# Kernel optimization log

Measured on AMD Instinct MI355X. Metric: run time of the kernel, lower is better.

Reference implementation:

```python
import jax, jax.numpy as jnp
import numpy as np

P = 100_000      # distinct products
T = 300_000      # total product nodes after repeat_interleave (sum of cnt)
NQ = 100_000     # query nodes
B = 8192         # number of sessions (segments)
QIN = 128; PIN = 128; D = 128; MSL = 50; DL = D - MSL


def setup_inputs() -> dict:
    key = jax.random.key(0)
    ks = jax.random.split(key, 12)
    # irregular repeat counts in {1..5}, tiled so sum == 3*P == T exactly (static shape)
    cnt = jnp.asarray(np.tile(np.array([1, 2, 3, 4, 5], np.int32), P // 5))
    s = 0.05
    return {
        "query_feat": jax.random.normal(ks[0], (NQ, QIN), jnp.float32),
        "product_feat": jax.random.normal(ks[1], (P, PIN), jnp.float32),
        "Wq": jax.random.normal(ks[2], (DL, QIN), jnp.float32) * s,
        "bq": jnp.zeros((DL,), jnp.float32),
        "Wp": jax.random.normal(ks[3], (DL, PIN), jnp.float32) * s,
        "bp": jnp.zeros((DL,), jnp.float32),
        "pos_table": jax.random.normal(ks[4], (MSL, MSL), jnp.float32) * s,
        "Wn": jax.random.normal(ks[5], (D, D), jnp.float32) * s,
        "bn": jnp.zeros((D,), jnp.float32),
        "Wc": jax.random.normal(ks[6], (D, D), jnp.float32) * s,
        "Wa": jax.random.normal(ks[7], (1, D), jnp.float32) * s,
        "query_pos_id": jax.random.randint(ks[8], (NQ,), 0, MSL, jnp.int32),
        "product_pos_id": jax.random.randint(ks[9], (T,), 0, MSL, jnp.int32),
        "query_batch": jax.random.randint(ks[10], (NQ,), 0, B, jnp.int32),
        "product_batch": jax.random.randint(ks[11], (P,), 0, B, jnp.int32),
        "cnt": cnt,
        "num_segments": B,
        "total_product_nodes": T,
    }


def _segment_mean(x, seg, num_segments):
    sums = jax.ops.segment_sum(x, seg, num_segments=num_segments)
    counts = jax.ops.segment_sum(jnp.ones((x.shape[0],), x.dtype), seg, num_segments=num_segments)
    return sums / jnp.maximum(counts, 1.0)[:, None]


def reference(query_feat, product_feat, Wq, bq, Wp, bp, pos_table, Wn, bn, Wc, Wa,
              query_pos_id, product_pos_id, query_batch, product_batch, cnt,
              num_segments, total_product_nodes):
    # query branch: linear -> concat positional embedding -> tanh  [NQ, D]
    qe = jnp.tanh(jnp.concatenate([query_feat @ Wq.T + bq, pos_table[query_pos_id]], axis=1))
    # product branch: linear, repeat_interleave by cnt, concat pos emb, tanh  [T, D]
    pe = product_feat @ Wp.T + bp
    pe = jnp.repeat(pe, cnt, axis=0, total_repeat_length=total_product_nodes)
    pe = jnp.tanh(jnp.concatenate([pe, pos_table[product_pos_id]], axis=1))
    pbatch = jnp.repeat(product_batch, cnt, axis=0, total_repeat_length=total_product_nodes)
    # stack nodes (products first, then queries — matches torch.concat order)
    node_emb = jnp.concatenate([pe, qe], axis=0)            # [N, D]
    node_batch = jnp.concatenate([pbatch, query_batch], axis=0)
    # coarse session representation: segment mean, broadcast back to nodes
    coarse = _segment_mean(node_emb, node_batch, num_segments)  # [B, D]
    coarse_g = coarse[node_batch]                                # [N, D]
    # attention gating
    att = jax.nn.sigmoid(node_emb @ Wn.T + bn + coarse_g @ Wc.T) @ Wa.T  # [N, 1]
    weighted = node_emb * att
    return _segment_mean(weighted, node_batch, num_segments)    # [B, D]
```

## Files before the change

kernel.cpp:

```cpp
#include <hip/hip_runtime.h>
#include <hip/hip_bf16.h>
#include <math.h>


constexpr int D   = 128;
constexpr int DL  = 78;
constexpr int MSL = 50;
constexpr int RP  = 80;

typedef __attribute__((ext_vector_type(8))) short bfrag8;
typedef __attribute__((ext_vector_type(4))) float facc4;
typedef __attribute__((ext_vector_type(4))) short short4v;

__device__ __forceinline__ float sigmoidf_(float x) {
    return 1.f / (1.f + __expf(-x));
}
__device__ __forceinline__ float ftanh(float x) {
    float e = __expf(2.f * x);
    return 1.f - 2.f * __builtin_amdgcn_rcpf(e + 1.f);
}

__device__ __forceinline__ char* ldsAddr(__hip_bfloat16* base, int row, int byte_in_row) {
    return reinterpret_cast<char*>(base) + row * 256 + (byte_in_row ^ ((row & 7) << 4));
}
__device__ __forceinline__ bfrag8 ldsR16(const __hip_bfloat16* base, int row, int byte_in_row) {
    return *reinterpret_cast<const bfrag8*>(
        reinterpret_cast<const char*>(base) + row * 256 + (byte_in_row ^ ((row & 7) << 4)));
}
__device__ __forceinline__ short4v ldsR8(const __hip_bfloat16* base, int row, int byte_in_row) {
    return *reinterpret_cast<const short4v*>(
        reinterpret_cast<const char*>(base) + row * 256 + (byte_in_row ^ ((row & 7) << 4)));
}

__device__ __forceinline__ bfrag8 cvt8(float4 a, float4 b) {
    __hip_bfloat16 t[8] = {__float2bfloat16(a.x), __float2bfloat16(a.y),
                           __float2bfloat16(a.z), __float2bfloat16(a.w),
                           __float2bfloat16(b.x), __float2bfloat16(b.y),
                           __float2bfloat16(b.z), __float2bfloat16(b.w)};
    return *reinterpret_cast<bfrag8*>(t);
}

__global__ __launch_bounds__(256) void k_tables2(
    const float* __restrict__ pos_table, const float* __restrict__ Wn,
    float* __restrict__ tpos, float* __restrict__ posWn) {
    __shared__ float tposL[MSL * MSL];
    int t = threadIdx.x;
    for (int o = t; o < MSL * MSL; o += 256) tposL[o] = tanhf(pos_table[o]);
    __syncthreads();
    if (blockIdx.x == 0)
        for (int o = t; o < MSL * MSL; o += 256) tpos[o] = tposL[o];
    for (int o = blockIdx.x * 256 + t; o < MSL * D; o += gridDim.x * 256) {
        int r = o >> 7, d = o & 127;
        float acc = 0.f;
        #pragma unroll 10
        for (int j = 0; j < MSL; ++j) acc += tposL[r * MSL + j] * Wn[d * D + DL + j];
        posWn[o] = acc;
    }
}

__global__ __launch_bounds__(256) void k_convW(
    const float* __restrict__ Wq, const float* __restrict__ Wp, const float* __restrict__ Wn,
    __hip_bfloat16* __restrict__ Wqbf, __hip_bfloat16* __restrict__ Wpbf,
    __hip_bfloat16* __restrict__ Wnbf) {
    int i = blockIdx.x * 256 + threadIdx.x;
    if (i < 80 * 128) {
        int n = i >> 7;
        Wqbf[i] = __float2bfloat16((n < DL) ? Wq[i] : 0.f);
        Wpbf[i] = __float2bfloat16((n < DL) ? Wp[i] : 0.f);
    } else if (i < 80 * 128 + 128 * 128) {
        int o = i - 80 * 128;
        int j = o & 127;
        Wnbf[o] = __float2bfloat16((j < DL) ? Wn[o] : 0.f);
    }
}

__global__ void k_scanA(const int* __restrict__ cnt, int P, int* __restrict__ chunkSum) {
    __shared__ int s[256];
    int p = blockIdx.x * 256 + threadIdx.x;
    s[threadIdx.x] = (p < P) ? cnt[p] : 0;
    __syncthreads();
    for (int st = 128; st > 0; st >>= 1) {
        if (threadIdx.x < st) s[threadIdx.x] += s[threadIdx.x + st];
        __syncthreads();
    }
    if (threadIdx.x == 0) chunkSum[blockIdx.x] = s[0];
}
__global__ __launch_bounds__(1024) void k_scanB(
    const int* __restrict__ chunkSum, int nC, int* __restrict__ chunkOff) {
    __shared__ int s[1024];
    int t = threadIdx.x;
    int carry = 0;
    for (int base = 0; base < nC; base += 1024) {
        int v = (base + t < nC) ? chunkSum[base + t] : 0;
        s[t] = v;
        __syncthreads();
        for (int st = 1; st < 1024; st <<= 1) {
            int add = (t >= st) ? s[t - st] : 0;
            __syncthreads();
            s[t] += add;
            __syncthreads();
        }
        if (base + t < nC) chunkOff[base + t] = carry + s[t] - v;
        carry += s[1023];
        __syncthreads();
    }
}
__global__ void k_scanC(const int* __restrict__ cnt, int P, const int* __restrict__ chunkOff,
                        int* __restrict__ prodOff) {
    __shared__ int s[256];
    int t = threadIdx.x;
    int p = blockIdx.x * 256 + t;
    int v = (p < P) ? cnt[p] : 0;
    s[t] = v;
    __syncthreads();
    for (int st = 1; st < 256; st <<= 1) {
        int add = (t >= st) ? s[t - st] : 0;
        __syncthreads();
        s[t] += add;
        __syncthreads();
    }
    if (p < P) prodOff[p] = chunkOff[blockIdx.x] + s[t] - v;
}

__global__ void k_nodecnt(const int* __restrict__ qbatch, const int* __restrict__ pbatch,
                          int NQ, int N, int* __restrict__ nodeCnt) {
    int r = blockIdx.x * 256 + threadIdx.x;
    if (r >= N) return;
    int b = (r < NQ) ? qbatch[r] : pbatch[r - NQ];
    atomicAdd(&nodeCnt[b], 1);
}
__global__ __launch_bounds__(1024) void k_scanSeg(
    const int* __restrict__ nodeCnt, int B, int* __restrict__ segOff, int* __restrict__ cursor) {
    __shared__ int s[1024];
    int t = threadIdx.x;
    int carry = 0;
    for (int base = 0; base < B; base += 1024) {
        int v = (base + t < B) ? nodeCnt[base + t] : 0;
        s[t] = v;
        __syncthreads();
        for (int st = 1; st < 1024; st <<= 1) {
            int add = (t >= st) ? s[t - st] : 0;
            __syncthreads();
            s[t] += add;
            __syncthreads();
        }
        if (base + t < B) {
            int e = carry + s[t] - v;
            segOff[base + t] = e;
            cursor[base + t] = e;
        }
        carry += s[1023];
        __syncthreads();
    }
    if (t == 0) segOff[B] = carry;
}
__global__ void k_rank(const int* __restrict__ qbatch, const int* __restrict__ pbatch,
                       int NQ, int N, int* __restrict__ cursor, int* __restrict__ rowOf) {
    int r = blockIdx.x * 256 + threadIdx.x;
    if (r >= N) return;
    int b = (r < NQ) ? qbatch[r] : pbatch[r - NQ];
    int slot = atomicAdd(&cursor[b], 1);
    rowOf[slot] = r;
}

__global__ __launch_bounds__(256) void k_branch2(
    const float* __restrict__ qfeat, const float* __restrict__ pfeat,
    const __hip_bfloat16* __restrict__ Wqbf, const __hip_bfloat16* __restrict__ Wpbf,
    const float* __restrict__ bq, const float* __restrict__ bp,
    const __hip_bfloat16* __restrict__ Wnbf,
    const int* __restrict__ qbatch, const int* __restrict__ pbatch,
    const int* __restrict__ qpos, const int* __restrict__ ppos,
    const int* __restrict__ cnt, const int* __restrict__ prodOff,
    int NQ, int P, int qBlocks,
    __hip_bfloat16* __restrict__ tq, __hip_bfloat16* __restrict__ tp,
    __hip_bfloat16* __restrict__ qWn, __hip_bfloat16* __restrict__ pWn,
    int* __restrict__ hist) {
    const bool isQ = (int)blockIdx.x < qBlocks;
    const int r0 = (isQ ? blockIdx.x : blockIdx.x - qBlocks) * 64;
    const float* feat = isQ ? qfeat : pfeat;
    const __hip_bfloat16* Wbf = isQ ? Wqbf : Wpbf;
    const float* bias = isQ ? bq : bp;
    const int* batch = isQ ? qbatch : pbatch;
    const int Nrows = isQ ? NQ : P;
    __hip_bfloat16* tE  = isQ ? tq : tp;
    __hip_bfloat16* eWn = isQ ? qWn : pWn;

    __shared__ __hip_bfloat16 linL[64 * 128];
    __shared__ __hip_bfloat16 eWnL[64 * 128];
    int t = threadIdx.x;
    int l = t & 63, w = t >> 6;
    int lr = l & 15, lq = l >> 4;
    int am = w * 16 + lr;

    if (l < 16) {
        bfrag8 z = {0, 0, 0, 0, 0, 0, 0, 0};
        *reinterpret_cast<bfrag8*>(ldsAddr(linL, w * 16 + l, 160)) = z;
        *reinterpret_cast<bfrag8*>(ldsAddr(linL, w * 16 + l, 176)) = z;
    }

    int gra = r0 + am;
    const float* frow = &feat[(size_t)(gra < Nrows ? gra : Nrows - 1) * 128];
    bfrag8 a[4];
    #pragma unroll
    for (int kt = 0; kt < 4; ++kt) {
        float4 u = *reinterpret_cast<const float4*>(&frow[kt * 32 + lq * 8]);
        float4 v = *reinterpret_cast<const float4*>(&frow[kt * 32 + lq * 8 + 4]);
        a[kt] = cvt8(u, v);
    }

    facc4 c1[5];
    #pragma unroll
    for (int nt = 0; nt < 5; ++nt) { facc4 z = {0.f, 0.f, 0.f, 0.f}; c1[nt] = z; }
    #pragma unroll
    for (int nt = 0; nt < 5; ++nt) {
        #pragma unroll
        for (int kt = 0; kt < 4; ++kt) {
            bfrag8 b = *reinterpret_cast<const bfrag8*>(&Wbf[(nt * 16 + lr) * 128 + kt * 32 + lq * 8]);
            c1[nt] = __builtin_amdgcn_mfma_f32_16x16x32_bf16(a[kt], b, c1[nt], 0, 0, 0);
        }
    }

    #pragma unroll
    for (int nt = 0; nt < 5; ++nt) {
        int n = nt * 16 + lr;
        float bs = (n < DL) ? bias[n] : 0.f;
        #pragma unroll
        for (int j = 0; j < 4; ++j) {
            int m = w * 16 + lq * 4 + j;
            float tv = (n < DL) ? ftanh(c1[nt][j] + bs) : 0.f;
            *reinterpret_cast<__hip_bfloat16*>(ldsAddr(linL, m, 2 * n)) = __float2bfloat16(tv);
        }
    }

    {
        int r = w * 16 + (l >> 2), c = l & 3;
        int gr = r0 + r;
        #pragma unroll
        for (int j = 0; j < 5; ++j) {
            short4v v = ldsR8(linL, r, c * 40 + j * 8);
            if (gr < Nrows)
                *reinterpret_cast<short4v*>(&tE[(size_t)gr * RP + c * 20 + j * 4]) = v;
        }
    }

    bfrag8 a2[3];
    #pragma unroll
    for (int kt = 0; kt < 3; ++kt) a2[kt] = ldsR16(linL, am, kt * 64 + lq * 16);
    facc4 c2[8];
    #pragma unroll
    for (int nt = 0; nt < 8; ++nt) { facc4 z = {0.f, 0.f, 0.f, 0.f}; c2[nt] = z; }
    #pragma unroll
    for (int nt = 0; nt < 8; ++nt) {
        #pragma unroll
        for (int kt = 0; kt < 3; ++kt) {
            bfrag8 b = *reinterpret_cast<const bfrag8*>(&Wnbf[(nt * 16 + lr) * 128 + kt * 32 + lq * 8]);
            c2[nt] = __builtin_amdgcn_mfma_f32_16x16x32_bf16(a2[kt], b, c2[nt], 0, 0, 0);
        }
    }
    #pragma unroll
    for (int nt = 0; nt < 8; ++nt) {
        int d2 = nt * 16 + lr;
        #pragma unroll
        for (int j = 0; j < 4; ++j) {
            int m = w * 16 + lq * 4 + j;
            *reinterpret_cast<__hip_bfloat16*>(ldsAddr(eWnL, m, 2 * d2)) =
                __float2bfloat16(c2[nt][j]);
        }
    }
    {
        int r = w * 16 + (l >> 2), c = l & 3;
        int gr = r0 + r;
        #pragma unroll
        for (int j = 0; j < 4; ++j) {
            bfrag8 v = ldsR16(eWnL, r, c * 64 + j * 16);
            if (gr < Nrows)
                *reinterpret_cast<bfrag8*>(&eWn[(size_t)gr * 128 + c * 32 + j * 8]) = v;
        }
    }

    if (t < 64) {
        int gr = r0 + t;
        if (gr < Nrows) {
            int b = batch[gr];
            if (isQ) {
                atomicAdd(&hist[b * MSL + qpos[gr]], 1);
            } else {
                int c = cnt[gr], off2 = prodOff[gr];
                for (int j = 0; j < c; ++j)
                    atomicAdd(&hist[b * MSL + ppos[off2 + j]], 1);
            }
        }
    }
}

__global__ __launch_bounds__(128) void k_segsum2(
    const __hip_bfloat16* __restrict__ tq, const __hip_bfloat16* __restrict__ tp,
    const int* __restrict__ cnt, const int* __restrict__ rowOf,
    const int* __restrict__ segOff, const int* __restrict__ hist,
    const float* __restrict__ tpos, int NQ,
    float* __restrict__ segsum, float* __restrict__ segcnt) {
    int b = blockIdx.x, t = threadIdx.x;
    if (t < DL) {
        int s0 = segOff[b], s1 = segOff[b + 1];
        float acc = 0.f;
        for (int i = s0; i < s1; ++i) {
            int r = rowOf[i];
            float wv, val;
            if (r < NQ) {
                wv = 1.f;
                val = __bfloat162float(tq[(size_t)r * RP + t]);
            } else {
                int pr = r - NQ;
                wv = (float)cnt[pr];
                val = __bfloat162float(tp[(size_t)pr * RP + t]);
            }
            acc += wv * val;
        }
        segsum[(size_t)b * D + t] = acc;
    } else {
        int k = t - DL;
        float acc = 0.f, c = 0.f;
        for (int r = 0; r < MSL; ++r) {
            float h = (float)hist[b * MSL + r];
            acc += h * tpos[r * MSL + k];
            c += h;
        }
        segsum[(size_t)b * D + DL + k] = acc;
        if (k == 0) segcnt[b] = c;
    }
}

__global__ __launch_bounds__(256) void k_coarse(
    const float* __restrict__ segsum, const float* __restrict__ segcnt,
    const float* __restrict__ Wc, const float* __restrict__ bn, int B,
    float* __restrict__ coarseWc) {
    __shared__ __hip_bfloat16 WcL[128 * 130];
    __shared__ float cL[16 * 128];
    int t = threadIdx.x;
    int b0 = blockIdx.x * 16;
    for (int o = t; o < D * D; o += 256) {
        int d = o >> 7, k = o & 127;
        WcL[d * 130 + k] = __float2bfloat16(Wc[o]);
    }
    for (int o = t; o < 16 * D; o += 256) {
        int bb = o >> 7, d = o & 127;
        int b = b0 + bb;
        cL[o] = (b < B) ? segsum[(size_t)b * D + d] / fmaxf(segcnt[b], 1.f) : 0.f;
    }
    __syncthreads();
    for (int o = t; o < 16 * D; o += 256) {
        int bb = o >> 7, d = o & 127;
        int b = b0 + bb;
        if (b >= B) continue;
        float acc = bn[d];
        const float* cr = &cL[bb * 128];
        const __hip_bfloat16* wr = &WcL[d * 130];
        #pragma unroll 8
        for (int j = 0; j < D; ++j) acc += cr[j] * __bfloat162float(wr[j]);
        coarseWc[(size_t)b * D + d] = acc;
    }
}

__global__ __launch_bounds__(256) void k_att3(
    const __hip_bfloat16* __restrict__ pWn, const __hip_bfloat16* __restrict__ tp,
    const __hip_bfloat16* __restrict__ qWn, const __hip_bfloat16* __restrict__ tq,
    const float* __restrict__ coarseWc, const float* __restrict__ posWn,
    const float* __restrict__ tpos, const float* __restrict__ Wa,
    const int* __restrict__ rowOf, const int* __restrict__ segOff,
    const int* __restrict__ prodOff, const int* __restrict__ cnt,
    const int* __restrict__ ppos, const int* __restrict__ qpos,
    const float* __restrict__ segcnt, int NQ, int B,
    float* __restrict__ out) {
    int wv = threadIdx.x >> 6, l = threadIdx.x & 63;
    int b = blockIdx.x * 4 + wv;
    if (b >= B) return;

    float cw0 = coarseWc[(size_t)b * D + l];
    float cw1 = coarseWc[(size_t)b * D + 64 + l];
    float wa0 = Wa[l], wa1 = Wa[64 + l];
    float acc0 = 0.f, acc1 = 0.f, posacc = 0.f;
    int s0 = segOff[b], s1 = segOff[b + 1];

    for (int i = s0; i < s1; ++i) {
        int r = rowOf[i];
        if (r < NQ) {
            int pos = qpos[r];
            float z0 = __bfloat162float(qWn[(size_t)r * D + l])      + cw0 + posWn[pos * D + l];
            float z1 = __bfloat162float(qWn[(size_t)r * D + 64 + l]) + cw1 + posWn[pos * D + 64 + l];
            float part = sigmoidf_(z0) * wa0 + sigmoidf_(z1) * wa1;
            #pragma unroll
            for (int m = 1; m < 64; m <<= 1) part += __shfl_xor(part, m, 64);
            acc0 += part * __bfloat162float(tq[(size_t)r * RP + l]);
            if (l < 14) acc1 += part * __bfloat162float(tq[(size_t)r * RP + 64 + l]);
            else posacc += part * tpos[pos * MSL + (l - 14)];
        } else {
            int p = r - NQ;
            int off = prodOff[p], c = cnt[p];
            float base0 = __bfloat162float(pWn[(size_t)p * D + l])      + cw0;
            float base1 = __bfloat162float(pWn[(size_t)p * D + 64 + l]) + cw1;
            float part[5];
            int   posr[5];
            #pragma unroll
            for (int j = 0; j < 5; ++j) {
                bool on = j < c;
                int pos = on ? ppos[off + j] : 0;
                posr[j] = pos;
                float z0 = base0 + posWn[pos * D + l];
                float z1 = base1 + posWn[pos * D + 64 + l];
                part[j] = on ? (sigmoidf_(z0) * wa0 + sigmoidf_(z1) * wa1) : 0.f;
            }
            #pragma unroll
            for (int m = 1; m < 64; m <<= 1) {
                #pragma unroll
                for (int j = 0; j < 5; ++j) part[j] += __shfl_xor(part[j], m, 64);
            }
            float attsum = part[0] + part[1] + part[2] + part[3] + part[4];
            if (l >= 14) {
                #pragma unroll
                for (int j = 0; j < 5; ++j)
                    posacc += part[j] * tpos[posr[j] * MSL + (l - 14)];
            }
            acc0 += attsum * __bfloat162float(tp[(size_t)p * RP + l]);
            if (l < 14) acc1 += attsum * __bfloat162float(tp[(size_t)p * RP + 64 + l]);
        }
    }

    float inv = 1.f / fmaxf(segcnt[b], 1.f);
    out[(size_t)b * D + l] = acc0 * inv;
    out[(size_t)b * D + 64 + l] = (l < 14 ? acc1 : posacc) * inv;
}

extern "C" void kernel_launch(void* const* d_in, const int* in_sizes, int n_in,
                              void* d_out, int out_size, void* d_ws, size_t ws_size,
                              hipStream_t stream) {
    const float* query_feat   = (const float*)d_in[0];
    const float* product_feat = (const float*)d_in[1];
    const float* Wq = (const float*)d_in[2];
    const float* bq = (const float*)d_in[3];
    const float* Wp = (const float*)d_in[4];
    const float* bp = (const float*)d_in[5];
    const float* pos_table = (const float*)d_in[6];
    const float* Wn = (const float*)d_in[7];
    const float* bn = (const float*)d_in[8];
    const float* Wc = (const float*)d_in[9];
    const float* Wa = (const float*)d_in[10];
    const int* qpos   = (const int*)d_in[11];
    const int* ppos   = (const int*)d_in[12];
    const int* qbatch = (const int*)d_in[13];
    const int* pbatch = (const int*)d_in[14];
    const int* cnt    = (const int*)d_in[15];

    int NQ = in_sizes[11];
    int P  = in_sizes[15];
    int B  = out_size / D;
    int N  = NQ + P;
    float* out = (float*)d_out;

    char* w = (char*)d_ws;
    size_t off = 0;
    auto take = [&](size_t bytes) -> char* {
        char* p = w + off;
        off = (off + bytes + 255) & ~(size_t)255;
        return p;
    };
    int*   hist    = (int*)  take((size_t)B * MSL * 4);
    int*   nodeCnt = (int*)  take((size_t)B * 4);
    size_t zeroBytes = off;
    float* segsum  = (float*)take((size_t)B * D * 4);
    float* segcnt   = (float*)take((size_t)B * 4);
    float* coarseWc = (float*)take((size_t)B * D * 4);
    float* tpos  = (float*)take(MSL * MSL * 4);
    float* posWn = (float*)take(MSL * D * 4);
    __hip_bfloat16* Wqbf = (__hip_bfloat16*)take(80 * 128 * 2);
    __hip_bfloat16* Wpbf = (__hip_bfloat16*)take(80 * 128 * 2);
    __hip_bfloat16* Wnbf = (__hip_bfloat16*)take(128 * 128 * 2);
    int nC = (P + 255) / 256;
    int* chunkSum = (int*)take((size_t)nC * 4);
    int* chunkOff = (int*)take((size_t)nC * 4);
    int* prodOff  = (int*)take((size_t)P * 4);
    int* segOffA  = (int*)take((size_t)(B + 1) * 4);
    int* cursor   = (int*)take((size_t)B * 4);
    int* rowOf    = (int*)take((size_t)N * 4);
    __hip_bfloat16* tq  = (__hip_bfloat16*)take((size_t)NQ * RP * 2);
    __hip_bfloat16* tp  = (__hip_bfloat16*)take((size_t)P * RP * 2);
    __hip_bfloat16* qWn = (__hip_bfloat16*)take((size_t)NQ * D * 2);
    __hip_bfloat16* pWn = (__hip_bfloat16*)take((size_t)P * D * 2);
    (void)ws_size; (void)n_in;

    hipMemsetAsync(hist, 0, zeroBytes, stream);

    hipLaunchKernelGGL(k_tables2, dim3(8), dim3(256), 0, stream, pos_table, Wn, tpos, posWn);
    hipLaunchKernelGGL(k_convW, dim3((80 * 128 + 128 * 128 + 255) / 256), dim3(256), 0, stream,
                       Wq, Wp, Wn, Wqbf, Wpbf, Wnbf);
    hipLaunchKernelGGL(k_scanA, dim3(nC), dim3(256), 0, stream, cnt, P, chunkSum);
    hipLaunchKernelGGL(k_scanB, dim3(1), dim3(1024), 0, stream, chunkSum, nC, chunkOff);
    hipLaunchKernelGGL(k_scanC, dim3(nC), dim3(256), 0, stream, cnt, P, chunkOff, prodOff);

    hipLaunchKernelGGL(k_nodecnt, dim3((N + 255) / 256), dim3(256), 0, stream,
                       qbatch, pbatch, NQ, N, nodeCnt);
    hipLaunchKernelGGL(k_scanSeg, dim3(1), dim3(1024), 0, stream, nodeCnt, B, segOffA, cursor);
    hipLaunchKernelGGL(k_rank, dim3((N + 255) / 256), dim3(256), 0, stream,
                       qbatch, pbatch, NQ, N, cursor, rowOf);

    int qBlocks = (NQ + 63) / 64, pBlocksBr = (P + 63) / 64;
    hipLaunchKernelGGL(k_branch2, dim3(qBlocks + pBlocksBr), dim3(256), 0, stream,
                       query_feat, product_feat, Wqbf, Wpbf, bq, bp, Wnbf,
                       qbatch, pbatch, qpos, ppos, cnt, prodOff, NQ, P, qBlocks,
                       tq, tp, qWn, pWn, hist);

    hipLaunchKernelGGL(k_segsum2, dim3(B), dim3(128), 0, stream,
                       tq, tp, cnt, rowOf, segOffA, hist, tpos, NQ, segsum, segcnt);
    hipLaunchKernelGGL(k_coarse, dim3((B + 15) / 16), dim3(256), 0, stream,
                       segsum, segcnt, Wc, bn, B, coarseWc);

    hipLaunchKernelGGL(k_att3, dim3((B + 3) / 4), dim3(256), 0, stream,
                       pWn, tp, qWn, tq, coarseWc, posWn, tpos, Wa,
                       rowOf, segOffA, prodOff, cnt, ppos, qpos, segcnt, NQ, B, out);
}
```

Before: 316.8 us.

## Expand nodes into packed row/pos index list, unify buffers, drop histogram

Replaces the per-row ordering with a per-node index array that packs the source row and position id, built while ranking nodes into segments. Query and product embeddings go into unified buffers, so the segment-sum and attention kernels run one branch-free loop with 8-way batching of shuffle reductions. The position histogram and its atomics in the branch kernel are removed, and segment counts come directly from the offsets. In exchange, product embeddings are re-read once per expanded node instead of once per product, and the index array is larger.

```diff
diff --git a/kernel.cpp b/kernel.cpp
--- a/kernel.cpp
+++ b/kernel.cpp
@@ -122,12 +122,15 @@
     if (p < P) prodOff[p] = chunkOff[blockIdx.x] + s[t] - v;
 }
 
-__global__ void k_nodecnt(const int* __restrict__ qbatch, const int* __restrict__ pbatch,
-                          int NQ, int N, int* __restrict__ nodeCnt) {
-    int r = blockIdx.x * 256 + threadIdx.x;
-    if (r >= N) return;
-    int b = (r < NQ) ? qbatch[r] : pbatch[r - NQ];
-    atomicAdd(&nodeCnt[b], 1);
+__global__ void k_cnt2(const int* __restrict__ qbatch, const int* __restrict__ pbatch,
+                       const int* __restrict__ cnt, int NQ, int P, int* __restrict__ nodeCnt) {
+    int i = blockIdx.x * 256 + threadIdx.x;
+    if (i < NQ) {
+        atomicAdd(&nodeCnt[qbatch[i]], 1);
+    } else if (i < NQ + P) {
+        int p = i - NQ;
+        atomicAdd(&nodeCnt[pbatch[p]], cnt[p]);
+    }
 }
 __global__ __launch_bounds__(1024) void k_scanSeg(
     const int* __restrict__ nodeCnt, int B, int* __restrict__ segOff, int* __restrict__ cursor) {
@@ -154,13 +157,21 @@
     }
     if (t == 0) segOff[B] = carry;
 }
-__global__ void k_rank(const int* __restrict__ qbatch, const int* __restrict__ pbatch,
-                       int NQ, int N, int* __restrict__ cursor, int* __restrict__ rowOf) {
-    int r = blockIdx.x * 256 + threadIdx.x;
-    if (r >= N) return;
-    int b = (r < NQ) ? qbatch[r] : pbatch[r - NQ];
-    int slot = atomicAdd(&cursor[b], 1);
-    rowOf[slot] = r;
+__global__ void k_rank2(const int* __restrict__ qbatch, const int* __restrict__ pbatch,
+                        const int* __restrict__ qpos, const int* __restrict__ ppos,
+                        const int* __restrict__ cnt, const int* __restrict__ prodOff,
+                        int NQ, int P, int* __restrict__ cursor, int* __restrict__ nodeIdx) {
+    int i = blockIdx.x * 256 + threadIdx.x;
+    if (i < NQ) {
+        int slot = atomicAdd(&cursor[qbatch[i]], 1);
+        nodeIdx[slot] = (i << 6) | qpos[i];
+    } else if (i < NQ + P) {
+        int p = i - NQ;
+        int c = cnt[p], off = prodOff[p];
+        int slot = atomicAdd(&cursor[pbatch[p]], c);
+        for (int j = 0; j < c; ++j)
+            nodeIdx[slot + j] = ((NQ + p) << 6) | ppos[off + j];
+    }
 }
 
 __global__ __launch_bounds__(256) void k_branch2(
@@ -168,22 +179,15 @@
     const __hip_bfloat16* __restrict__ Wqbf, const __hip_bfloat16* __restrict__ Wpbf,
     const float* __restrict__ bq, const float* __restrict__ bp,
     const __hip_bfloat16* __restrict__ Wnbf,
-    const int* __restrict__ qbatch, const int* __restrict__ pbatch,
-    const int* __restrict__ qpos, const int* __restrict__ ppos,
-    const int* __restrict__ cnt, const int* __restrict__ prodOff,
     int NQ, int P, int qBlocks,
-    __hip_bfloat16* __restrict__ tq, __hip_bfloat16* __restrict__ tp,
-    __hip_bfloat16* __restrict__ qWn, __hip_bfloat16* __restrict__ pWn,
-    int* __restrict__ hist) {
+    __hip_bfloat16* __restrict__ tEU, __hip_bfloat16* __restrict__ eWnU) {
     const bool isQ = (int)blockIdx.x < qBlocks;
     const int r0 = (isQ ? blockIdx.x : blockIdx.x - qBlocks) * 64;
     const float* feat = isQ ? qfeat : pfeat;
     const __hip_bfloat16* Wbf = isQ ? Wqbf : Wpbf;
     const float* bias = isQ ? bq : bp;
-    const int* batch = isQ ? qbatch : pbatch;
     const int Nrows = isQ ? NQ : P;
-    __hip_bfloat16* tE  = isQ ? tq : tp;
-    __hip_bfloat16* eWn = isQ ? qWn : pWn;
+    const int rowBase = isQ ? 0 : NQ;
 
     __shared__ __hip_bfloat16 linL[64 * 128];
     __shared__ __hip_bfloat16 eWnL[64 * 128];
@@ -239,7 +243,7 @@
         for (int j = 0; j < 5; ++j) {
             short4v v = ldsR8(linL, r, c * 40 + j * 8);
             if (gr < Nrows)
-                *reinterpret_cast<short4v*>(&tE[(size_t)gr * RP + c * 20 + j * 4]) = v;
+                *reinterpret_cast<short4v*>(&tEU[(size_t)(rowBase + gr) * RP + c * 20 + j * 4]) = v;
         }
     }
 
@@ -274,59 +278,42 @@
         for (int j = 0; j < 4; ++j) {
             bfrag8 v = ldsR16(eWnL, r, c * 64 + j * 16);
             if (gr < Nrows)
-                *reinterpret_cast<bfrag8*>(&eWn[(size_t)gr * 128 + c * 32 + j * 8]) = v;
-        }
-    }
-
-    if (t < 64) {
-        int gr = r0 + t;
-        if (gr < Nrows) {
-            int b = batch[gr];
-            if (isQ) {
-                atomicAdd(&hist[b * MSL + qpos[gr]], 1);
-            } else {
-                int c = cnt[gr], off2 = prodOff[gr];
-                for (int j = 0; j < c; ++j)
-                    atomicAdd(&hist[b * MSL + ppos[off2 + j]], 1);
-            }
-        }
-    }
-}
-
-__global__ __launch_bounds__(128) void k_segsum2(
-    const __hip_bfloat16* __restrict__ tq, const __hip_bfloat16* __restrict__ tp,
-    const int* __restrict__ cnt, const int* __restrict__ rowOf,
-    const int* __restrict__ segOff, const int* __restrict__ hist,
-    const float* __restrict__ tpos, int NQ,
+                *reinterpret_cast<bfrag8*>(&eWnU[(size_t)(rowBase + gr) * 128 + c * 32 + j * 8]) = v;
+        }
+    }
+}
+
+__global__ __launch_bounds__(128) void k_segsum3(
+    const __hip_bfloat16* __restrict__ tEU, const int* __restrict__ nodeIdx,
+    const int* __restrict__ segOff, const float* __restrict__ tpos, int B,
     float* __restrict__ segsum, float* __restrict__ segcnt) {
     int b = blockIdx.x, t = threadIdx.x;
+    int s0 = segOff[b], s1 = segOff[b + 1];
+    float acc = 0.f;
     if (t < DL) {
-        int s0 = segOff[b], s1 = segOff[b + 1];
-        float acc = 0.f;
-        for (int i = s0; i < s1; ++i) {
-            int r = rowOf[i];
-            float wv, val;
-            if (r < NQ) {
-                wv = 1.f;
-                val = __bfloat162float(tq[(size_t)r * RP + t]);
-            } else {
-                int pr = r - NQ;
-                wv = (float)cnt[pr];
-                val = __bfloat162float(tp[(size_t)pr * RP + t]);
+        for (int i = s0; i < s1; i += 4) {
+            #pragma unroll
+            for (int j = 0; j < 4; ++j) {
+                if (i + j < s1) {
+                    int row = nodeIdx[i + j] >> 6;
+                    acc += __bfloat162float(tEU[(size_t)row * RP + t]);
+                }
             }
-            acc += wv * val;
         }
         segsum[(size_t)b * D + t] = acc;
     } else {
         int k = t - DL;
-        float acc = 0.f, c = 0.f;
-        for (int r = 0; r < MSL; ++r) {
-            float h = (float)hist[b * MSL + r];
-            acc += h * tpos[r * MSL + k];
-            c += h;
+        for (int i = s0; i < s1; i += 4) {
+            #pragma unroll
+            for (int j = 0; j < 4; ++j) {
+                if (i + j < s1) {
+                    int pos = nodeIdx[i + j] & 63;
+                    acc += tpos[pos * MSL + k];
+                }
+            }
         }
         segsum[(size_t)b * D + DL + k] = acc;
-        if (k == 0) segcnt[b] = c;
+        if (k == 0) segcnt[b] = (float)(s1 - s0);
     }
 }
 
@@ -361,16 +348,12 @@
     }
 }
 
-__global__ __launch_bounds__(256) void k_att3(
-    const __hip_bfloat16* __restrict__ pWn, const __hip_bfloat16* __restrict__ tp,
-    const __hip_bfloat16* __restrict__ qWn, const __hip_bfloat16* __restrict__ tq,
+__global__ __launch_bounds__(256) void k_att4(
+    const __hip_bfloat16* __restrict__ eWnU, const __hip_bfloat16* __restrict__ tEU,
     const float* __restrict__ coarseWc, const float* __restrict__ posWn,
     const float* __restrict__ tpos, const float* __restrict__ Wa,
-    const int* __restrict__ rowOf, const int* __restrict__ segOff,
-    const int* __restrict__ prodOff, const int* __restrict__ cnt,
-    const int* __restrict__ ppos, const int* __restrict__ qpos,
-    const float* __restrict__ segcnt, int NQ, int B,
-    float* __restrict__ out) {
+    const int* __restrict__ nodeIdx, const int* __restrict__ segOff,
+    const float* __restrict__ segcnt, int B, float* __restrict__ out) {
     int wv = threadIdx.x >> 6, l = threadIdx.x & 63;
     int b = blockIdx.x * 4 + wv;
     if (b >= B) return;
@@ -381,47 +364,29 @@
     float acc0 = 0.f, acc1 = 0.f, posacc = 0.f;
     int s0 = segOff[b], s1 = segOff[b + 1];
 
-    for (int i = s0; i < s1; ++i) {
-        int r = rowOf[i];
-        if (r < NQ) {
-            int pos = qpos[r];
-            float z0 = __bfloat162float(qWn[(size_t)r * D + l])      + cw0 + posWn[pos * D + l];
-            float z1 = __bfloat162float(qWn[(size_t)r * D + 64 + l]) + cw1 + posWn[pos * D + 64 + l];
-            float part = sigmoidf_(z0) * wa0 + sigmoidf_(z1) * wa1;
+    for (int i = s0; i < s1; i += 8) {
+        float part[8];
+        int   row[8], pos[8];
+        #pragma unroll
+        for (int j = 0; j < 8; ++j) {
+            bool on = (i + j) < s1;
+            int pk = on ? nodeIdx[i + j] : 0;
+            row[j] = pk >> 6;
+            pos[j] = pk & 63;
+            float z0 = __bfloat162float(eWnU[(size_t)row[j] * D + l])      + cw0 + posWn[pos[j] * D + l];
+            float z1 = __bfloat162float(eWnU[(size_t)row[j] * D + 64 + l]) + cw1 + posWn[pos[j] * D + 64 + l];
+            part[j] = on ? (sigmoidf_(z0) * wa0 + sigmoidf_(z1) * wa1) : 0.f;
+        }
+        #pragma unroll
+        for (int m = 1; m < 64; m <<= 1) {
             #pragma unroll
-            for (int m = 1; m < 64; m <<= 1) part += __shfl_xor(part, m, 64);
-            acc0 += part * __bfloat162float(tq[(size_t)r * RP + l]);
-            if (l < 14) acc1 += part * __bfloat162float(tq[(size_t)r * RP + 64 + l]);
-            else posacc += part * tpos[pos * MSL + (l - 14)];
-        } else {
-            int p = r - NQ;
-            int off = prodOff[p], c = cnt[p];
-            float base0 = __bfloat162float(pWn[(size_t)p * D + l])      + cw0;
-            float base1 = __bfloat162float(pWn[(size_t)p * D + 64 + l]) + cw1;
-            float part[5];
-            int   posr[5];
-            #pragma unroll
-            for (int j = 0; j < 5; ++j) {
-                bool on = j < c;
-                int pos = on ? ppos[off + j] : 0;
-                posr[j] = pos;
-                float z0 = base0 + posWn[pos * D + l];
-                float z1 = base1 + posWn[pos * D + 64 + l];
-                part[j] = on ? (sigmoidf_(z0) * wa0 + sigmoidf_(z1) * wa1) : 0.f;
-            }
-            #pragma unroll
-            for (int m = 1; m < 64; m <<= 1) {
-                #pragma unroll
-                for (int j = 0; j < 5; ++j) part[j] += __shfl_xor(part[j], m, 64);
-            }
-            float attsum = part[0] + part[1] + part[2] + part[3] + part[4];
-            if (l >= 14) {
-                #pragma unroll
-                for (int j = 0; j < 5; ++j)
-                    posacc += part[j] * tpos[posr[j] * MSL + (l - 14)];
-            }
-            acc0 += attsum * __bfloat162float(tp[(size_t)p * RP + l]);
-            if (l < 14) acc1 += attsum * __bfloat162float(tp[(size_t)p * RP + 64 + l]);
+            for (int j = 0; j < 8; ++j) part[j] += __shfl_xor(part[j], m, 64);
+        }
+        #pragma unroll
+        for (int j = 0; j < 8; ++j) {
+            acc0 += part[j] * __bfloat162float(tEU[(size_t)row[j] * RP + l]);
+            if (l < 14) acc1 += part[j] * __bfloat162float(tEU[(size_t)row[j] * RP + 64 + l]);
+            else        posacc += part[j] * tpos[pos[j] * MSL + (l - 14)];
         }
     }
 
@@ -451,9 +416,11 @@
     const int* cnt    = (const int*)d_in[15];
 
     int NQ = in_sizes[11];
+    int T  = in_sizes[12];
     int P  = in_sizes[15];
     int B  = out_size / D;
-    int N  = NQ + P;
+    int NR = NQ + P;
+    int NN = NQ + T;
     float* out = (float*)d_out;
 
     char* w = (char*)d_ws;
@@ -463,10 +430,9 @@
         off = (off + bytes + 255) & ~(size_t)255;
         return p;
     };
-    int*   hist    = (int*)  take((size_t)B * MSL * 4);
     int*   nodeCnt = (int*)  take((size_t)B * 4);
     size_t zeroBytes = off;
-    float* segsum  = (float*)take((size_t)B * D * 4);
+    float* segsum   = (float*)take((size_t)B * D * 4);
     float* segcnt   = (float*)take((size_t)B * 4);
     float* coarseWc = (float*)take((size_t)B * D * 4);
     float* tpos  = (float*)take(MSL * MSL * 4);
@@ -480,14 +446,12 @@
     int* prodOff  = (int*)take((size_t)P * 4);
     int* segOffA  = (int*)take((size_t)(B + 1) * 4);
     int* cursor   = (int*)take((size_t)B * 4);
-    int* rowOf    = (int*)take((size_t)N * 4);
-    __hip_bfloat16* tq  = (__hip_bfloat16*)take((size_t)NQ * RP * 2);
-    __hip_bfloat16* tp  = (__hip_bfloat16*)take((size_t)P * RP * 2);
-    __hip_bfloat16* qWn = (__hip_bfloat16*)take((size_t)NQ * D * 2);
-    __hip_bfloat16* pWn = (__hip_bfloat16*)take((size_t)P * D * 2);
+    int* nodeIdx  = (int*)take((size_t)NN * 4);
+    __hip_bfloat16* tEU  = (__hip_bfloat16*)take((size_t)NR * RP * 2);
+    __hip_bfloat16* eWnU = (__hip_bfloat16*)take((size_t)NR * D * 2);
     (void)ws_size; (void)n_in;
 
-    hipMemsetAsync(hist, 0, zeroBytes, stream);
+    hipMemsetAsync(nodeCnt, 0, zeroBytes, stream);
 
     hipLaunchKernelGGL(k_tables2, dim3(8), dim3(256), 0, stream, pos_table, Wn, tpos, posWn);
     hipLaunchKernelGGL(k_convW, dim3((80 * 128 + 128 * 128 + 255) / 256), dim3(256), 0, stream,
@@ -496,24 +460,23 @@
     hipLaunchKernelGGL(k_scanB, dim3(1), dim3(1024), 0, stream, chunkSum, nC, chunkOff);
     hipLaunchKernelGGL(k_scanC, dim3(nC), dim3(256), 0, stream, cnt, P, chunkOff, prodOff);
 
-    hipLaunchKernelGGL(k_nodecnt, dim3((N + 255) / 256), dim3(256), 0, stream,
-                       qbatch, pbatch, NQ, N, nodeCnt);
+    hipLaunchKernelGGL(k_cnt2, dim3((NR + 255) / 256), dim3(256), 0, stream,
+                       qbatch, pbatch, cnt, NQ, P, nodeCnt);
     hipLaunchKernelGGL(k_scanSeg, dim3(1), dim3(1024), 0, stream, nodeCnt, B, segOffA, cursor);
-    hipLaunchKernelGGL(k_rank, dim3((N + 255) / 256), dim3(256), 0, stream,
-                       qbatch, pbatch, NQ, N, cursor, rowOf);
+    hipLaunchKernelGGL(k_rank2, dim3((NR + 255) / 256), dim3(256), 0, stream,
+                       qbatch, pbatch, qpos, ppos, cnt, prodOff, NQ, P, cursor, nodeIdx);
 
     int qBlocks = (NQ + 63) / 64, pBlocksBr = (P + 63) / 64;
     hipLaunchKernelGGL(k_branch2, dim3(qBlocks + pBlocksBr), dim3(256), 0, stream,
                        query_feat, product_feat, Wqbf, Wpbf, bq, bp, Wnbf,
-                       qbatch, pbatch, qpos, ppos, cnt, prodOff, NQ, P, qBlocks,
-                       tq, tp, qWn, pWn, hist);
-
-    hipLaunchKernelGGL(k_segsum2, dim3(B), dim3(128), 0, stream,
-                       tq, tp, cnt, rowOf, segOffA, hist, tpos, NQ, segsum, segcnt);
+                       NQ, P, qBlocks, tEU, eWnU);
+
+    hipLaunchKernelGGL(k_segsum3, dim3(B), dim3(128), 0, stream,
+                       tEU, nodeIdx, segOffA, tpos, B, segsum, segcnt);
     hipLaunchKernelGGL(k_coarse, dim3((B + 15) / 16), dim3(256), 0, stream,
                        segsum, segcnt, Wc, bn, B, coarseWc);
 
-    hipLaunchKernelGGL(k_att3, dim3((B + 3) / 4), dim3(256), 0, stream,
-                       pWn, tp, qWn, tq, coarseWc, posWn, tpos, Wa,
-                       rowOf, segOffA, prodOff, cnt, ppos, qpos, segcnt, NQ, B, out);
-}
+    hipLaunchKernelGGL(k_att4, dim3((B + 3) / 4), dim3(256), 0, stream,
+                       eWnU, tEU, coarseWc, posWn, tpos, Wa,
+                       nodeIdx, segOffA, segcnt, B, out);
+}
```

Measured after the change: 377.9 us. +19.3%, slower.
